# Optimization experiments

Measured on AMD Instinct MI355X. Metric: run time of the kernel, lower is better.

Reference implementation:

```python
import jax, jax.numpy as jnp
import numpy as np

N = 8192; NFEAT = 1024; NHID = 256; NCLS = 16; DECAY = 0.9; EXPO = 3


def _ggcn_layer(h, adj, deg, W, b, deg_coeff, coeff, scale):
    # degree gate: softplus(a*deg + b), elementwise on [N, N]
    sc = jax.nn.softplus(deg_coeff[0] * deg + deg_coeff[1])
    Wh = h @ W.T + b                           # [N, d_out]
    prod = Wh @ Wh.T                           # [N, N]
    sq = jnp.diag(prod)[:, None]               # squared norms [N, 1]
    e = prod / jnp.maximum(jnp.sqrt(sq * sq.T), 1e-9)   # cosine similarity
    n = e.shape[0]
    idx = jnp.arange(n)
    e = e.at[idx, idx].set(0.0)                # remove diagonal
    att = e * adj * sc
    att_pos = jax.nn.relu(att)
    att_neg = -jax.nn.relu(-att)
    c = jax.nn.softmax(coeff)
    s = jax.nn.softplus(scale)
    return s * (c[0] * (att_pos @ Wh) + c[1] * (att_neg @ Wh) + c[2] * Wh)


def _linear_params(k, out_f, in_f):
    k1, k2 = jax.random.split(k)
    W = jax.random.normal(k1, (out_f, in_f), jnp.float32) * (1.0 / np.sqrt(in_f))
    b = jax.random.normal(k2, (out_f,), jnp.float32) * 0.01
    return W, b


def setup_inputs() -> dict:
    key = jax.random.key(0)
    ks = jax.random.split(key, 8)
    x = jax.random.normal(ks[0], (N, NFEAT), jnp.float32)
    mask = (jax.random.uniform(ks[1], (N, N)) < 0.005).astype(jnp.float32)
    adj = mask + jnp.eye(N, dtype=jnp.float32)
    fcn_W, fcn_b = _linear_params(ks[2], NHID, NFEAT)
    W0, b0 = _linear_params(ks[3], NHID, NFEAT)
    W1, b1 = _linear_params(ks[4], NHID, NHID)
    W2, b2 = _linear_params(ks[5], NCLS, NHID)
    dc = jnp.array([0.5, 0.0], jnp.float32)   # deg_coeff init (use_decay=True)
    co = jnp.zeros((3,), jnp.float32)          # sign-mixing coeff init
    sl = 2.0 * jnp.ones((1,), jnp.float32)     # scale init (use_decay=True)
    return dict(x=x, adj=adj, fcn_W=fcn_W, fcn_b=fcn_b,
                W0=W0, b0=b0, dc0=dc, c0=co, s0=sl,
                W1=W1, b1=b1, dc1=dc, c1=co, s1=sl,
                W2=W2, b2=b2, dc2=dc, c2=co, s2=sl,
                test_idx=0)


def reference(x, adj, fcn_W, fcn_b,
              W0, b0, dc0, c0, s0,
              W1, b1, dc1, c1, s1,
              W2, b2, dc2, c2, s2,
              test_idx):
    # precompute_degree_d: diag(adj)/max(adj,1e-9) - 1
    deg = jnp.diag(adj)[:, None] / jnp.maximum(adj, 1e-9) - 1.0
    prev = jax.nn.elu(x @ fcn_W.T + fcn_b)
    inner = _ggcn_layer(x, adj, deg, W0, b0, dc0, c0, s0)
    # loop iter i=0
    inner = jax.nn.elu(inner)
    prev = inner + prev
    inner = _ggcn_layer(prev, adj, deg, W1, b1, dc1, c1, s1)
    # loop iter i=1 (decay coeff, i+2 = 3)
    inner = jax.nn.elu(inner)
    decay_coeff = float(np.log(DECAY / (3 ** EXPO) + 1.0))
    prev = decay_coeff * inner + prev
    inner = _ggcn_layer(prev, adj, deg, W2, b2, dc2, c2, s2)
    logp = jax.nn.log_softmax(inner, axis=1)
    pred = jax.nn.softmax(inner, axis=1)
    top2, _ = jax.lax.top_k(pred, 2)
    calib = jnp.mean(top2[:, 0] + top2[:, 1])
    return (logp, calib, pred)
```

## Files before the change

kernel.cpp:

```cpp
#include <hip/hip_runtime.h>
#include <math.h>

#define NN 8192
#define NFEAT 1024
#define NHID 256
#define NCLS 16
#define ELLW 128

typedef unsigned short u16;
typedef __bf16 bf16x8 __attribute__((ext_vector_type(8)));
typedef float f32x4 __attribute__((ext_vector_type(4)));

__device__ __forceinline__ float u2f(u16 h) {
    union { unsigned int u; float f; } x; x.u = ((unsigned int)h) << 16; return x.f;
}
__device__ __forceinline__ u16 f2b(float f) {
    union { float f; unsigned int u; } x; x.f = f;
    unsigned int r = x.u + 0x7FFFu + ((x.u >> 16) & 1u);
    return (u16)(r >> 16);
}
__device__ __forceinline__ float softplusf(float x) {
    return (x > 20.f) ? x : log1pf(expf(x));
}
__device__ __forceinline__ float eluf(float x) {
    return x > 0.f ? x : expm1f(x);
}
__device__ __forceinline__ float ldsc(const void* p, int k, int F) {
    return F ? ((const float*)p)[k] : u2f(((const u16*)p)[k]);
}

__global__ __launch_bounds__(64) void k_detect(const unsigned int* __restrict__ x32,
                                               int* __restrict__ flag)
{
    const int t = threadIdx.x;
    unsigned int maxe = 0; int nz = 0;
    #pragma unroll
    for (int q = 0; q < 4; q++) {
        unsigned int w = x32[t * 4 + q];
        unsigned int e = (w >> 7) & 0xFFu;
        maxe = maxe > e ? maxe : e;
        nz += ((w & 0xFFFFu) == 0u) ? 1 : 0;
    }
    #pragma unroll
    for (int off = 32; off >= 1; off >>= 1) {
        unsigned int me = __shfl_xor(maxe, off);
        maxe = maxe > me ? maxe : me;
        nz += __shfl_xor(nz, off);
    }
    if (t == 0) flag[0] = (maxe > 0x90u || nz > 128) ? 1 : 0;
}

__global__ __launch_bounds__(256) void k_extract(
    const void* __restrict__ adjp, u16* __restrict__ eidx, u16* __restrict__ eadjh,
    u16* __restrict__ edegh, int* __restrict__ cnt, const int* __restrict__ dflag)
{
    const int F = dflag[0];
    const int i = blockIdx.x;
    const int t = threadIdx.x;
    __shared__ int scnt;
    if (t == 0) scnt = 0;
    float aii = F ? ((const float*)adjp)[(size_t)i * NN + i]
                  : u2f(((const u16*)adjp)[(size_t)i * NN + i]);
    __syncthreads();
    for (int b = 0; b < 4; b++) {
        int j0 = b * 2048 + t * 8;
        float va[8];
        if (F) {
            const float* g = (const float*)adjp + (size_t)i * NN + j0;
            float4 f0 = ((const float4*)g)[0];
            float4 f1 = ((const float4*)g)[1];
            va[0] = f0.x; va[1] = f0.y; va[2] = f0.z; va[3] = f0.w;
            va[4] = f1.x; va[5] = f1.y; va[6] = f1.z; va[7] = f1.w;
        } else {
            const u16* g = (const u16*)adjp + (size_t)i * NN + j0;
            uint4 v = *(const uint4*)g;
            unsigned int ws4[4] = { v.x, v.y, v.z, v.w };
            #pragma unroll
            for (int q = 0; q < 4; q++) {
                va[q * 2]     = u2f((u16)(ws4[q] & 0xFFFFu));
                va[q * 2 + 1] = u2f((u16)(ws4[q] >> 16));
            }
        }
        #pragma unroll
        for (int q = 0; q < 8; q++) {
            int j = j0 + q;
            if (va[q] != 0.f && j != i) {
                int p = atomicAdd(&scnt, 1);
                if (p < ELLW) {
                    eidx[(size_t)i * ELLW + p] = (u16)j;
                    eadjh[(size_t)i * ELLW + p] = f2b(va[q]);
                    edegh[(size_t)i * ELLW + p] = f2b(aii / fmaxf(va[q], 1e-9f) - 1.0f);
                }
            }
        }
    }
    __syncthreads();
    if (t == 0) cnt[i] = (scnt < ELLW) ? scnt : ELLW;
}

__global__ __launch_bounds__(256) void k_gemm(
    const void* __restrict__ Ap, int a_f32, const void* __restrict__ Bp,
    const void* __restrict__ biasp, float* __restrict__ C,
    int N, int K, int flags, const int* __restrict__ dflag)
{
    const int F = dflag[0];
    const bool af = (a_f32 != 0) || (F != 0);
    const bool bf = (F != 0);
    const int LDT = 40;
    __shared__ __align__(16) u16 Ah[128 * 40];
    __shared__ __align__(16) u16 Al[128 * 40];
    __shared__ __align__(16) u16 Bh[128 * 40];
    __shared__ __align__(16) u16 Bl[128 * 40];
    const int t = threadIdx.x;
    const int m0 = blockIdx.x * 128;
    const int n0 = blockIdx.y * 128;
    const int lane = t & 63, wv = t >> 6;
    const int quad = lane >> 4, lr = lane & 15;
    const int wr0 = (wv >> 1) * 64, wc0 = (wv & 1) * 64;

    f32x4 acc[4][4];
    #pragma unroll
    for (int a = 0; a < 4; a++)
        #pragma unroll
        for (int b = 0; b < 4; b++) acc[a][b] = f32x4{0.f, 0.f, 0.f, 0.f};

    const int sr = t >> 1;
    const int sk = (t & 1) * 16;

    for (int kt = 0; kt < K; kt += 32) {
        if (af) {
            const float* g = (const float*)Ap + (size_t)(m0 + sr) * K + kt + sk;
            float4 f0 = ((const float4*)g)[0];
            float4 f1 = ((const float4*)g)[1];
            float4 f2 = ((const float4*)g)[2];
            float4 f3 = ((const float4*)g)[3];
            float va[16] = { f0.x, f0.y, f0.z, f0.w, f1.x, f1.y, f1.z, f1.w,
                             f2.x, f2.y, f2.z, f2.w, f3.x, f3.y, f3.z, f3.w };
            #pragma unroll
            for (int q = 0; q < 16; q++) {
                u16 h = f2b(va[q]);
                Ah[sr * LDT + sk + q] = h;
                Al[sr * LDT + sk + q] = f2b(va[q] - u2f(h));
            }
        } else {
            const u16* g = (const u16*)Ap + (size_t)(m0 + sr) * K + kt + sk;
            *(uint4*)&Ah[sr * LDT + sk]     = ((const uint4*)g)[0];
            *(uint4*)&Ah[sr * LDT + sk + 8] = ((const uint4*)g)[1];
        }
        if (bf) {
            const float* g = (const float*)Bp + (size_t)(n0 + sr) * K + kt + sk;
            float4 f0 = ((const float4*)g)[0];
            float4 f1 = ((const float4*)g)[1];
            float4 f2 = ((const float4*)g)[2];
            float4 f3 = ((const float4*)g)[3];
            float vb[16] = { f0.x, f0.y, f0.z, f0.w, f1.x, f1.y, f1.z, f1.w,
                             f2.x, f2.y, f2.z, f2.w, f3.x, f3.y, f3.z, f3.w };
            #pragma unroll
            for (int q = 0; q < 16; q++) {
                u16 h = f2b(vb[q]);
                Bh[sr * LDT + sk + q] = h;
                Bl[sr * LDT + sk + q] = f2b(vb[q] - u2f(h));
            }
        } else {
            const u16* g = (const u16*)Bp + (size_t)(n0 + sr) * K + kt + sk;
            *(uint4*)&Bh[sr * LDT + sk]     = ((const uint4*)g)[0];
            *(uint4*)&Bh[sr * LDT + sk + 8] = ((const uint4*)g)[1];
        }
        __syncthreads();
        bf16x8 ah[4], bh[4];
        #pragma unroll
        for (int mt = 0; mt < 4; mt++)
            ah[mt] = *(const bf16x8*)&Ah[(wr0 + mt * 16 + lr) * LDT + quad * 8];
        #pragma unroll
        for (int nt = 0; nt < 4; nt++)
            bh[nt] = *(const bf16x8*)&Bh[(wc0 + nt * 16 + lr) * LDT + quad * 8];
        #pragma unroll
        for (int mt = 0; mt < 4; mt++)
            #pragma unroll
            for (int nt = 0; nt < 4; nt++)
                acc[mt][nt] = __builtin_amdgcn_mfma_f32_16x16x32_bf16(ah[mt], bh[nt], acc[mt][nt], 0, 0, 0);
        if (af) {
            bf16x8 al[4];
            #pragma unroll
            for (int mt = 0; mt < 4; mt++)
                al[mt] = *(const bf16x8*)&Al[(wr0 + mt * 16 + lr) * LDT + quad * 8];
            #pragma unroll
            for (int mt = 0; mt < 4; mt++)
                #pragma unroll
                for (int nt = 0; nt < 4; nt++)
                    acc[mt][nt] = __builtin_amdgcn_mfma_f32_16x16x32_bf16(al[mt], bh[nt], acc[mt][nt], 0, 0, 0);
        }
        if (bf) {
            bf16x8 bl[4];
            #pragma unroll
            for (int nt = 0; nt < 4; nt++)
                bl[nt] = *(const bf16x8*)&Bl[(wc0 + nt * 16 + lr) * LDT + quad * 8];
            #pragma unroll
            for (int mt = 0; mt < 4; mt++)
                #pragma unroll
                for (int nt = 0; nt < 4; nt++)
                    acc[mt][nt] = __builtin_amdgcn_mfma_f32_16x16x32_bf16(ah[mt], bl[nt], acc[mt][nt], 0, 0, 0);
        }
        __syncthreads();
    }

    #pragma unroll
    for (int mt = 0; mt < 4; mt++) {
        #pragma unroll
        for (int nt = 0; nt < 4; nt++) {
            int col = n0 + wc0 + nt * 16 + lr;
            float bsv = (flags & 1) ? ldsc(biasp, col, F) : 0.f;
            #pragma unroll
            for (int r = 0; r < 4; r++) {
                int rowi = m0 + wr0 + mt * 16 + quad * 4 + r;
                float v = acc[mt][nt][r] + bsv;
                if (flags & 2) v = eluf(v);
                C[(size_t)rowi * N + col] = v;
            }
        }
    }
}

__global__ __launch_bounds__(256) void k_rownorm(const float* __restrict__ Wh, float* __restrict__ nrm)
{
    const int t = threadIdx.x;
    const int lane = t & 63, wv = t >> 6;
    const int row = blockIdx.x * 4 + wv;
    float4 v = *(const float4*)&Wh[(size_t)row * NHID + lane * 4];
    float p = v.x * v.x + v.y * v.y + v.z * v.z + v.w * v.w;
    #pragma unroll
    for (int off = 32; off >= 1; off >>= 1) p += __shfl_xor(p, off);
    if (lane == 0) nrm[row] = sqrtf(p);
}

__global__ __launch_bounds__(256) void k_spmm(
    const float* __restrict__ Wh, const float* __restrict__ nrm,
    const u16* __restrict__ eidx, const u16* __restrict__ eadjh, const u16* __restrict__ edegh,
    const int* __restrict__ cnt,
    const void* __restrict__ dc, const void* __restrict__ cv, const void* __restrict__ sv,
    float alpha, float* __restrict__ prev, const int* __restrict__ dflag)
{
    const int F = dflag[0];
    __shared__ __align__(16) float whi[NHID];
    __shared__ __align__(16) float wvals[ELLW];
    __shared__ __align__(16) int   jind[ELLW];
    const int i = blockIdx.x, t = threadIdx.x;
    whi[t] = Wh[(size_t)i * NHID + t];
    float e0 = expf(ldsc(cv, 0, F)), e1 = expf(ldsc(cv, 1, F)), e2 = expf(ldsc(cv, 2, F));
    float esum = e0 + e1 + e2;
    float c0 = e0 / esum, c1 = e1 / esum, c2 = e2 / esum;
    float s = softplusf(ldsc(sv, 0, F));
    float d0 = ldsc(dc, 0, F), d1 = ldsc(dc, 1, F);
    float ni = nrm[i];
    int n = cnt[i];
    if (n > ELLW) n = ELLW;
    if (n < 0) n = 0;
    __syncthreads();
    const int lane = t & 63, wvv = t >> 6;
    for (int e = wvv; e < n; e += 4) {
        int j = (int)eidx[(size_t)i * ELLW + e] & (NN - 1);
        float4 wj = *(const float4*)&Wh[(size_t)j * NHID + lane * 4];
        float4 wi = *(const float4*)&whi[lane * 4];
        float p = wj.x * wi.x + wj.y * wi.y + wj.z * wi.z + wj.w * wi.w;
        #pragma unroll
        for (int off = 32; off >= 1; off >>= 1) p += __shfl_xor(p, off);
        if (lane == 0) {
            float denom = fmaxf(ni * nrm[j], 1e-9f);
            float ecos = p / denom;
            float sc = softplusf(d0 * u2f(edegh[(size_t)i * ELLW + e]) + d1);
            float att = ecos * u2f(eadjh[(size_t)i * ELLW + e]) * sc;
            wvals[e] = c0 * fmaxf(att, 0.f) + c1 * fminf(att, 0.f);
            jind[e] = j;
        }
    }
    __syncthreads();
    float acc = 0.f;
    for (int e = 0; e < n; e++)
        acc += wvals[e] * Wh[(size_t)jind[e] * NHID + t];
    float o = s * (acc + c2 * whi[t]);
    float inner = eluf(o);
    size_t off = (size_t)i * NHID + t;
    prev[off] = alpha * inner + prev[off];
}

__global__ __launch_bounds__(256) void k_gemm16(
    const float* __restrict__ Af, const void* __restrict__ W2p, const void* __restrict__ b2p,
    float* __restrict__ Wh2, const int* __restrict__ dflag)
{
    const int F = dflag[0];
    __shared__ __align__(16) float Asf[16 * 256];
    __shared__ __align__(16) float Wsf[16 * 256];
    const int t = threadIdx.x;
    const int i0 = blockIdx.x * 16;
    const int sr = t >> 4, soff = (t & 15) * 16;
    #pragma unroll
    for (int q = 0; q < 4; q++)
        *(float4*)&Asf[sr * 256 + soff + q * 4] = *(const float4*)&Af[(size_t)(i0 + sr) * 256 + soff + q * 4];
    if (F) {
        const float* g = (const float*)W2p + (size_t)sr * 256 + soff;
        #pragma unroll
        for (int q = 0; q < 4; q++)
            *(float4*)&Wsf[sr * 256 + soff + q * 4] = ((const float4*)g)[q];
    } else {
        const u16* g = (const u16*)W2p + (size_t)sr * 256 + soff;
        uint4 h0 = ((const uint4*)g)[0];
        uint4 h1 = ((const uint4*)g)[1];
        unsigned int ws8[8] = { h0.x, h0.y, h0.z, h0.w, h1.x, h1.y, h1.z, h1.w };
        #pragma unroll
        for (int q = 0; q < 8; q++) {
            Wsf[sr * 256 + soff + q * 2]     = u2f((u16)(ws8[q] & 0xFFFFu));
            Wsf[sr * 256 + soff + q * 2 + 1] = u2f((u16)(ws8[q] >> 16));
        }
    }
    __syncthreads();
    const int r = t >> 4, c = t & 15;
    float acc = ldsc(b2p, c, F);
    for (int k = 0; k < 256; k++)
        acc += Asf[r * 256 + k] * Wsf[c * 256 + k];
    Wh2[(size_t)(i0 + r) * 16 + c] = acc;
}

__global__ __launch_bounds__(256) void k_norm16(const float* __restrict__ Wh2, float* __restrict__ nrm2)
{
    int i = blockIdx.x * blockDim.x + threadIdx.x;
    if (i >= NN) return;
    float s = 0.f;
    #pragma unroll
    for (int k = 0; k < 16; k++) { float v = Wh2[(size_t)i * 16 + k]; s += v * v; }
    nrm2[i] = sqrtf(s);
}

__global__ __launch_bounds__(64) void k_final(
    const float* __restrict__ Wh2, const float* __restrict__ nrm2,
    const u16* __restrict__ eidx, const u16* __restrict__ eadjh, const u16* __restrict__ edegh,
    const int* __restrict__ cnt,
    const void* __restrict__ dc, const void* __restrict__ cv, const void* __restrict__ sv,
    void* __restrict__ outp, float* __restrict__ calib, const int* __restrict__ dflag)
{
    const int F = dflag[0];
    __shared__ __align__(16) float w2i[16];
    __shared__ __align__(16) float wvals[ELLW];
    __shared__ __align__(16) int   jind[ELLW];
    __shared__ __align__(16) float lg[16];
    __shared__ float sh_lse;
    const int i = blockIdx.x, t = threadIdx.x;
    if (t < 16) w2i[t] = Wh2[(size_t)i * 16 + t];
    float e0 = expf(ldsc(cv, 0, F)), e1 = expf(ldsc(cv, 1, F)), e2 = expf(ldsc(cv, 2, F));
    float esum = e0 + e1 + e2;
    float c0 = e0 / esum, c1 = e1 / esum, c2 = e2 / esum;
    float s = softplusf(ldsc(sv, 0, F));
    float d0 = ldsc(dc, 0, F), d1 = ldsc(dc, 1, F);
    float ni = nrm2[i];
    int n = cnt[i];
    if (n > ELLW) n = ELLW;
    if (n < 0) n = 0;
    __syncthreads();
    for (int e = t; e < n; e += 64) {
        int j = (int)eidx[(size_t)i * ELLW + e] & (NN - 1);
        float p = 0.f;
        #pragma unroll
        for (int k = 0; k < 16; k++) p += w2i[k] * Wh2[(size_t)j * 16 + k];
        float denom = fmaxf(ni * nrm2[j], 1e-9f);
        float sc = softplusf(d0 * u2f(edegh[(size_t)i * ELLW + e]) + d1);
        float att = (p / denom) * u2f(eadjh[(size_t)i * ELLW + e]) * sc;
        wvals[e] = c0 * fmaxf(att, 0.f) + c1 * fminf(att, 0.f);
        jind[e] = j;
    }
    __syncthreads();
    if (t < 16) {
        float acc = 0.f;
        for (int e = 0; e < n; e++) acc += wvals[e] * Wh2[(size_t)jind[e] * 16 + t];
        lg[t] = s * (acc + c2 * w2i[t]);
    }
    __syncthreads();
    if (t == 0) {
        float m1 = -1e30f, m2 = -1e30f;
        for (int k = 0; k < 16; k++) {
            float v = lg[k];
            if (v > m1) { m2 = m1; m1 = v; } else if (v > m2) m2 = v;
        }
        float sum = 0.f;
        for (int k = 0; k < 16; k++) sum += expf(lg[k] - m1);
        float lse = m1 + logf(sum);
        sh_lse = lse;
        atomicAdd(calib, expf(m1 - lse) + expf(m2 - lse));
    }
    __syncthreads();
    if (t < 16) {
        float lp = lg[t] - sh_lse;
        if (F) {
            float* of = (float*)outp;
            of[(size_t)i * 16 + t] = lp;
            of[131073 + (size_t)i * 16 + t] = expf(lp);
        } else {
            u16* oh = (u16*)outp;
            oh[(size_t)i * 16 + t] = f2b(lp);
            oh[131073 + (size_t)i * 16 + t] = f2b(expf(lp));
        }
    }
}

__global__ void k_calib(const float* __restrict__ calib, void* __restrict__ outp,
                        const int* __restrict__ dflag)
{
    float v = calib[0] * (1.0f / 8192.0f);
    if (dflag[0]) ((float*)outp)[131072] = v;
    else ((u16*)outp)[131072] = f2b(v);
}

extern "C" void kernel_launch(void* const* d_in, const int* in_sizes, int n_in,
                              void* d_out, int out_size, void* d_ws, size_t ws_size,
                              hipStream_t stream)
{
    const void* x     = d_in[0];
    const void* adj   = d_in[1];
    const void* fcn_W = d_in[2];
    const void* fcn_b = d_in[3];
    const void* W0    = d_in[4];
    const void* b0    = d_in[5];
    const void* dc0   = d_in[6];
    const void* c0    = d_in[7];
    const void* s0    = d_in[8];
    const void* W1    = d_in[9];
    const void* b1    = d_in[10];
    const void* dc1   = d_in[11];
    const void* c1    = d_in[12];
    const void* s1    = d_in[13];
    const void* W2    = d_in[14];
    const void* b2    = d_in[15];
    const void* dc2   = d_in[16];
    const void* c2    = d_in[17];
    const void* s2    = d_in[18];

    char* w = (char*)d_ws;
    int*   dflag  = (int*)w;    w += 256;
    u16*   eidx   = (u16*)w;    w += (size_t)NN * ELLW * 2;
    u16*   eadjh  = (u16*)w;    w += (size_t)NN * ELLW * 2;
    u16*   edegh  = (u16*)w;    w += (size_t)NN * ELLW * 2;
    int*   cnt    = (int*)w;    w += NN * 4;
    float* prev   = (float*)w;  w += (size_t)NN * NHID * 4;
    float* Wh     = (float*)w;  w += (size_t)NN * NHID * 4;
    float* nrm    = (float*)w;  w += NN * 4;
    float* Wh2    = (float*)w;  w += (size_t)NN * NCLS * 4;
    float* nrm2   = (float*)w;  w += NN * 4;
    float* calib  = (float*)w;  w += 256;

    const float DECAYC = 0.0327898222829908f;

    k_detect<<<1, 64, 0, stream>>>((const unsigned int*)x, dflag);
    k_extract<<<NN, 256, 0, stream>>>(adj, eidx, eadjh, edegh, cnt, dflag);
    k_gemm<<<dim3(NN / 128, NHID / 128), 256, 0, stream>>>(x, 0, fcn_W, fcn_b, prev, NHID, NFEAT, 1 | 2, dflag);
    k_gemm<<<dim3(NN / 128, NHID / 128), 256, 0, stream>>>(x, 0, W0, b0, Wh, NHID, NFEAT, 1, dflag);
    k_rownorm<<<NN / 4, 256, 0, stream>>>(Wh, nrm);
    k_spmm<<<NN, 256, 0, stream>>>(Wh, nrm, eidx, eadjh, edegh, cnt, dc0, c0, s0, 1.0f, prev, dflag);
    k_gemm<<<dim3(NN / 128, NHID / 128), 256, 0, stream>>>(prev, 1, W1, b1, Wh, NHID, NHID, 1, dflag);
    k_rownorm<<<NN / 4, 256, 0, stream>>>(Wh, nrm);
    k_spmm<<<NN, 256, 0, stream>>>(Wh, nrm, eidx, eadjh, edegh, cnt, dc1, c1, s1, DECAYC, prev, dflag);
    k_gemm16<<<NN / 16, 256, 0, stream>>>(prev, W2, b2, Wh2, dflag);
    k_norm16<<<NN / 256, 256, 0, stream>>>(Wh2, nrm2);
    hipMemsetAsync(calib, 0, sizeof(float), stream);
    k_final<<<NN, 64, 0, stream>>>(Wh2, nrm2, eidx, eadjh, edegh, cnt, dc2, c2, s2, d_out, calib, dflag);
    k_calib<<<1, 1, 0, stream>>>(calib, d_out, dflag);
}
```

Baseline: 974.6 us.

## Fuse SpMM gather into edge loop, merge x GEMMs, fold norms and memset

The SpMM kernel now accumulates the weighted neighbour rows directly in the edge loop, reusing the already-gathered Wh row. This replaces the separate second gather pass and the lane-0 serial scoring, at the cost of a cross-wave LDS reduction. The two GEMMs that read x are merged into one launch, the 16-wide row norm is computed inside k_gemm16, and the calib memset moves into k_detect. k_final now uses 256 threads with 16-lane groups per edge, which removes launches and serial per-edge work.

Result: faster. 874.6 us (-10.3%).

```diff
diff --git a/kernel.cpp b/kernel.cpp
--- a/kernel.cpp
+++ b/kernel.cpp
@@ -30,7 +30,8 @@
 }
 
 __global__ __launch_bounds__(64) void k_detect(const unsigned int* __restrict__ x32,
-                                               int* __restrict__ flag)
+                                               int* __restrict__ flag,
+                                               float* __restrict__ calib)
 {
     const int t = threadIdx.x;
     unsigned int maxe = 0; int nz = 0;
@@ -47,7 +48,10 @@
         maxe = maxe > me ? maxe : me;
         nz += __shfl_xor(nz, off);
     }
-    if (t == 0) flag[0] = (maxe > 0x90u || nz > 128) ? 1 : 0;
+    if (t == 0) {
+        flag[0] = (maxe > 0x90u || nz > 128) ? 1 : 0;
+        calib[0] = 0.f;
+    }
 }
 
 __global__ __launch_bounds__(256) void k_extract(
@@ -98,22 +102,17 @@
     if (t == 0) cnt[i] = (scnt < ELLW) ? scnt : ELLW;
 }
 
-__global__ __launch_bounds__(256) void k_gemm(
-    const void* __restrict__ Ap, int a_f32, const void* __restrict__ Bp,
+__device__ __forceinline__ void gemm_body(
+    const void* __restrict__ Ap, bool af, const void* __restrict__ Bp, bool bf,
     const void* __restrict__ biasp, float* __restrict__ C,
-    int N, int K, int flags, const int* __restrict__ dflag)
-{
-    const int F = dflag[0];
-    const bool af = (a_f32 != 0) || (F != 0);
-    const bool bf = (F != 0);
+    int m0, int n0, int N, int K, int flags, int F)
+{
     const int LDT = 40;
     __shared__ __align__(16) u16 Ah[128 * 40];
     __shared__ __align__(16) u16 Al[128 * 40];
     __shared__ __align__(16) u16 Bh[128 * 40];
     __shared__ __align__(16) u16 Bl[128 * 40];
     const int t = threadIdx.x;
-    const int m0 = blockIdx.x * 128;
-    const int n0 = blockIdx.y * 128;
     const int lane = t & 63, wv = t >> 6;
     const int quad = lane >> 4, lr = lane & 15;
     const int wr0 = (wv >> 1) * 64, wc0 = (wv & 1) * 64;
@@ -221,6 +220,34 @@
     }
 }
 
+__global__ __launch_bounds__(256) void k_gemm(
+    const void* __restrict__ Ap, int a_f32, const void* __restrict__ Bp,
+    const void* __restrict__ biasp, float* __restrict__ C,
+    int N, int K, int flags, const int* __restrict__ dflag)
+{
+    const int F = dflag[0];
+    gemm_body(Ap, (a_f32 != 0) || (F != 0), Bp, F != 0, biasp, C,
+              blockIdx.x * 128, blockIdx.y * 128, N, K, flags, F);
+}
+
+__global__ __launch_bounds__(256) void k_gemm_x(
+    const void* __restrict__ x,
+    const void* __restrict__ fcnW, const void* __restrict__ fcnb,
+    const void* __restrict__ W0, const void* __restrict__ b0,
+    float* __restrict__ prev, float* __restrict__ Wh,
+    const int* __restrict__ dflag)
+{
+    const int F = dflag[0];
+    const int sel = blockIdx.y >> 1;
+    const int n0 = (blockIdx.y & 1) * 128;
+    const void* B = sel ? W0 : fcnW;
+    const void* bs = sel ? b0 : fcnb;
+    float* C = sel ? Wh : prev;
+    const int flags = sel ? 1 : 3;
+    gemm_body(x, F != 0, B, F != 0, bs, C,
+              blockIdx.x * 128, n0, NHID, NFEAT, flags, F);
+}
+
 __global__ __launch_bounds__(256) void k_rownorm(const float* __restrict__ Wh, float* __restrict__ nrm)
 {
     const int t = threadIdx.x;
@@ -242,8 +269,7 @@
 {
     const int F = dflag[0];
     __shared__ __align__(16) float whi[NHID];
-    __shared__ __align__(16) float wvals[ELLW];
-    __shared__ __align__(16) int   jind[ELLW];
+    __shared__ __align__(16) float red[4][NHID];
     const int i = blockIdx.x, t = threadIdx.x;
     whi[t] = Wh[(size_t)i * NHID + t];
     float e0 = expf(ldsc(cv, 0, F)), e1 = expf(ldsc(cv, 1, F)), e2 = expf(ldsc(cv, 2, F));
@@ -257,35 +283,36 @@
     if (n < 0) n = 0;
     __syncthreads();
     const int lane = t & 63, wvv = t >> 6;
+    const float4 wi = *(const float4*)&whi[lane * 4];
+    f32x4 acc = {0.f, 0.f, 0.f, 0.f};
     for (int e = wvv; e < n; e += 4) {
         int j = (int)eidx[(size_t)i * ELLW + e] & (NN - 1);
         float4 wj = *(const float4*)&Wh[(size_t)j * NHID + lane * 4];
-        float4 wi = *(const float4*)&whi[lane * 4];
         float p = wj.x * wi.x + wj.y * wi.y + wj.z * wi.z + wj.w * wi.w;
         #pragma unroll
         for (int off = 32; off >= 1; off >>= 1) p += __shfl_xor(p, off);
-        if (lane == 0) {
-            float denom = fmaxf(ni * nrm[j], 1e-9f);
-            float ecos = p / denom;
-            float sc = softplusf(d0 * u2f(edegh[(size_t)i * ELLW + e]) + d1);
-            float att = ecos * u2f(eadjh[(size_t)i * ELLW + e]) * sc;
-            wvals[e] = c0 * fmaxf(att, 0.f) + c1 * fminf(att, 0.f);
-            jind[e] = j;
-        }
-    }
-    __syncthreads();
-    float acc = 0.f;
-    for (int e = 0; e < n; e++)
-        acc += wvals[e] * Wh[(size_t)jind[e] * NHID + t];
-    float o = s * (acc + c2 * whi[t]);
+        float denom = fmaxf(ni * nrm[j], 1e-9f);
+        float ecos = p / denom;
+        float sc = softplusf(d0 * u2f(edegh[(size_t)i * ELLW + e]) + d1);
+        float att = ecos * u2f(eadjh[(size_t)i * ELLW + e]) * sc;
+        float wval = c0 * fmaxf(att, 0.f) + c1 * fminf(att, 0.f);
+        acc[0] += wval * wj.x;
+        acc[1] += wval * wj.y;
+        acc[2] += wval * wj.z;
+        acc[3] += wval * wj.w;
+    }
+    *(f32x4*)&red[wvv][lane * 4] = acc;
+    __syncthreads();
+    float tot = red[0][t] + red[1][t] + red[2][t] + red[3][t];
+    float o = s * (tot + c2 * whi[t]);
     float inner = eluf(o);
-    size_t off = (size_t)i * NHID + t;
-    prev[off] = alpha * inner + prev[off];
+    size_t off2 = (size_t)i * NHID + t;
+    prev[off2] = alpha * inner + prev[off2];
 }
 
 __global__ __launch_bounds__(256) void k_gemm16(
     const float* __restrict__ Af, const void* __restrict__ W2p, const void* __restrict__ b2p,
-    float* __restrict__ Wh2, const int* __restrict__ dflag)
+    float* __restrict__ Wh2, float* __restrict__ nrm2, const int* __restrict__ dflag)
 {
     const int F = dflag[0];
     __shared__ __align__(16) float Asf[16 * 256];
@@ -318,19 +345,13 @@
     for (int k = 0; k < 256; k++)
         acc += Asf[r * 256 + k] * Wsf[c * 256 + k];
     Wh2[(size_t)(i0 + r) * 16 + c] = acc;
-}
-
-__global__ __launch_bounds__(256) void k_norm16(const float* __restrict__ Wh2, float* __restrict__ nrm2)
-{
-    int i = blockIdx.x * blockDim.x + threadIdx.x;
-    if (i >= NN) return;
-    float s = 0.f;
-    #pragma unroll
-    for (int k = 0; k < 16; k++) { float v = Wh2[(size_t)i * 16 + k]; s += v * v; }
-    nrm2[i] = sqrtf(s);
-}
-
-__global__ __launch_bounds__(64) void k_final(
+    float ss = acc * acc;
+    ss += __shfl_xor(ss, 1); ss += __shfl_xor(ss, 2);
+    ss += __shfl_xor(ss, 4); ss += __shfl_xor(ss, 8);
+    if (c == 0) nrm2[i0 + r] = sqrtf(ss);
+}
+
+__global__ __launch_bounds__(256) void k_final(
     const float* __restrict__ Wh2, const float* __restrict__ nrm2,
     const u16* __restrict__ eidx, const u16* __restrict__ eadjh, const u16* __restrict__ edegh,
     const int* __restrict__ cnt,
@@ -339,11 +360,12 @@
 {
     const int F = dflag[0];
     __shared__ __align__(16) float w2i[16];
-    __shared__ __align__(16) float wvals[ELLW];
-    __shared__ __align__(16) int   jind[ELLW];
+    __shared__ __align__(16) float red[4][16];
     __shared__ __align__(16) float lg[16];
     __shared__ float sh_lse;
     const int i = blockIdx.x, t = threadIdx.x;
+    const int lane = t & 63, wv = t >> 6;
+    const int g = lane >> 4, lc = lane & 15;
     if (t < 16) w2i[t] = Wh2[(size_t)i * 16 + t];
     float e0 = expf(ldsc(cv, 0, F)), e1 = expf(ldsc(cv, 1, F)), e2 = expf(ldsc(cv, 2, F));
     float esum = e0 + e1 + e2;
@@ -355,22 +377,28 @@
     if (n > ELLW) n = ELLW;
     if (n < 0) n = 0;
     __syncthreads();
-    for (int e = t; e < n; e += 64) {
+    const float wic = w2i[lc];
+    float acc = 0.f;
+    const int grp = wv * 4 + g;
+    for (int e = grp; e < n; e += 16) {
         int j = (int)eidx[(size_t)i * ELLW + e] & (NN - 1);
-        float p = 0.f;
-        #pragma unroll
-        for (int k = 0; k < 16; k++) p += w2i[k] * Wh2[(size_t)j * 16 + k];
+        float vj = Wh2[(size_t)j * 16 + lc];
+        float p = vj * wic;
+        p += __shfl_xor(p, 1); p += __shfl_xor(p, 2);
+        p += __shfl_xor(p, 4); p += __shfl_xor(p, 8);
         float denom = fmaxf(ni * nrm2[j], 1e-9f);
         float sc = softplusf(d0 * u2f(edegh[(size_t)i * ELLW + e]) + d1);
         float att = (p / denom) * u2f(eadjh[(size_t)i * ELLW + e]) * sc;
-        wvals[e] = c0 * fmaxf(att, 0.f) + c1 * fminf(att, 0.f);
-        jind[e] = j;
-    }
+        float wval = c0 * fmaxf(att, 0.f) + c1 * fminf(att, 0.f);
+        acc += wval * vj;
+    }
+    acc += __shfl_xor(acc, 16);
+    acc += __shfl_xor(acc, 32);
+    if (lane < 16) red[wv][lane] = acc;
     __syncthreads();
     if (t < 16) {
-        float acc = 0.f;
-        for (int e = 0; e < n; e++) acc += wvals[e] * Wh2[(size_t)jind[e] * 16 + t];
-        lg[t] = s * (acc + c2 * w2i[t]);
+        float tot = red[0][t] + red[1][t] + red[2][t] + red[3][t];
+        lg[t] = s * (tot + c2 * w2i[t]);
     }
     __syncthreads();
     if (t == 0) {
@@ -447,18 +475,15 @@
 
     const float DECAYC = 0.0327898222829908f;
 
-    k_detect<<<1, 64, 0, stream>>>((const unsigned int*)x, dflag);
+    k_detect<<<1, 64, 0, stream>>>((const unsigned int*)x, dflag, calib);
     k_extract<<<NN, 256, 0, stream>>>(adj, eidx, eadjh, edegh, cnt, dflag);
-    k_gemm<<<dim3(NN / 128, NHID / 128), 256, 0, stream>>>(x, 0, fcn_W, fcn_b, prev, NHID, NFEAT, 1 | 2, dflag);
-    k_gemm<<<dim3(NN / 128, NHID / 128), 256, 0, stream>>>(x, 0, W0, b0, Wh, NHID, NFEAT, 1, dflag);
+    k_gemm_x<<<dim3(NN / 128, 4), 256, 0, stream>>>(x, fcn_W, fcn_b, W0, b0, prev, Wh, dflag);
     k_rownorm<<<NN / 4, 256, 0, stream>>>(Wh, nrm);
     k_spmm<<<NN, 256, 0, stream>>>(Wh, nrm, eidx, eadjh, edegh, cnt, dc0, c0, s0, 1.0f, prev, dflag);
     k_gemm<<<dim3(NN / 128, NHID / 128), 256, 0, stream>>>(prev, 1, W1, b1, Wh, NHID, NHID, 1, dflag);
     k_rownorm<<<NN / 4, 256, 0, stream>>>(Wh, nrm);
     k_spmm<<<NN, 256, 0, stream>>>(Wh, nrm, eidx, eadjh, edegh, cnt, dc1, c1, s1, DECAYC, prev, dflag);
-    k_gemm16<<<NN / 16, 256, 0, stream>>>(prev, W2, b2, Wh2, dflag);
-    k_norm16<<<NN / 256, 256, 0, stream>>>(Wh2, nrm2);
-    hipMemsetAsync(calib, 0, sizeof(float), stream);
-    k_final<<<NN, 64, 0, stream>>>(Wh2, nrm2, eidx, eadjh, edegh, cnt, dc2, c2, s2, d_out, calib, dflag);
+    k_gemm16<<<NN / 16, 256, 0, stream>>>(prev, W2, b2, Wh2, nrm2, dflag);
+    k_final<<<NN, 256, 0, stream>>>(Wh2, nrm2, eidx, eadjh, edegh, cnt, dc2, c2, s2, d_out, calib, dflag);
     k_calib<<<1, 1, 0, stream>>>(calib, d_out, dflag);
 }
```
